# Kernel optimization log

Hardware: AMD Instinct MI355X
Metric: run time of the kernel (lower is better)

The kernel has to match this reference:

```python
import jax, jax.numpy as jnp
import numpy as np

SQRT2 = 1.41421356237
BASE_SCALE = 0.001
CDF_X = 10.0


def erf_poly(x):
    # Abramowitz-Stegun polynomial erf, exactly as the torch source
    sign = jnp.where(x > 0, 1.0, -1.0)  # torch: (x > 0) * 2 - 1
    x = jnp.abs(x)
    a1, a2, a3, a4, a5 = 0.254829592, -0.284496736, 1.421413741, -1.453152027, 1.061405429
    p = 0.3275911
    t = 1.0 / (1.0 + p * x)
    y = 1.0 - ((((a5 * t + a4) * t + a3) * t + a2) * t + a1) * t * jnp.exp(-x * x)
    return sign * y


def rot6d_to_rotmat(x):
    # Zhou et al. 6D rotation: Gram-Schmidt two columns, cross for third
    a1, a2 = x[..., :3], x[..., 3:6]
    b1 = a1 / jnp.linalg.norm(a1, axis=-1, keepdims=True)
    b2 = a2 - jnp.sum(b1 * a2, axis=-1, keepdims=True) * b1
    b2 = b2 / jnp.linalg.norm(b2, axis=-1, keepdims=True)
    b3 = jnp.cross(b1, b2)
    return jnp.stack([b1, b2, b3], axis=-1)  # columns b1,b2,b3 -> [..., 3, 3]


def setup_inputs() -> dict:
    key = jax.random.key(0)
    k1, k2, k3, k4 = jax.random.split(key, 4)
    R, B, G = 65536, 24, 4
    return {
        "w2ls": jax.random.normal(k1, (R, B, 4, 4), dtype=jnp.float32),
        "rays_o": jax.random.normal(k2, (R, 3), dtype=jnp.float32),
        "rays_d": jax.random.normal(k3, (R, 3), dtype=jnp.float32),
        "Gs": jax.random.normal(k4, (B, G, 13), dtype=jnp.float32),
        "N_unique": 1,
    }


def reference(w2ls, rays_o, rays_d, Gs, N_unique):
    # Gs-derived quantities are detached in the original get_1D_gaussians
    Gs = jax.lax.stop_gradient(Gs)
    R = rays_o.shape[0]
    dt = rays_o.dtype

    origins = jnp.concatenate([rays_o, jnp.ones((R, 1), dt)], axis=1)      # [r,4]
    dirs = jnp.concatenate([rays_d, jnp.zeros((R, 1), dt)], axis=1)        # [r,4]
    o = jnp.einsum('rbij,rj->rbi', w2ls, origins)[..., :3]                 # [r,b,3]
    n = jnp.einsum('rbij,rj->rbi', w2ls, dirs)[..., :3]                    # [r,b,3]

    G_mu = Gs[..., 0:3]                                                    # [b,g,3]
    G_std = jnp.abs(Gs[..., 3:6]) + BASE_SCALE                             # [b,g,3]
    G_R = rot6d_to_rotmat(Gs[..., 6:12])                                   # [b,g,3,3]
    G_c = jnp.abs(Gs[..., 12])                                             # [b,g]

    # S = diag(1/std); SR = S @ R scales rows of R
    SR = G_R / G_std[..., None]                                            # [b,g,3,3]
    Sn1 = jnp.einsum('bgki,bgkj->bgij', SR, SR)                            # R^T S^2 R

    mu_d_o = G_mu[None] - o[:, :, None, :]                                 # [r,b,g,3]
    nSn = jnp.einsum('rbi,bgij,rbj->rbg', n, Sn1, n)                       # n^T Sn1 n
    sigma_bar_sqr = 1.0 / nSn                                              # [r,b,g]
    mu_bar = jnp.einsum('rbi,bgij,rbgj->rbg', n, Sn1, mu_d_o) * sigma_bar_sqr
    quad = jnp.einsum('rbgi,bgij,rbgj->rbg', mu_d_o, Sn1, mu_d_o)

    densities = G_c[None] * jnp.exp(-0.5 * (quad - mu_bar ** 2 / sigma_bar_sqr))
    means = mu_bar
    sigmas = jnp.sqrt(sigma_bar_sqr)

    # soft density filter (weights computed on detached means)
    w = jax.nn.sigmoid(100.0 * jax.lax.stop_gradient(means) - 1.0)
    densities = densities * w

    # gaussian1d_cdf at x = 10.0, then shadow map: sum over all (bone, gaussian)
    cdf = densities * 0.5 * (1.0 + erf_poly((CDF_X - means) / (sigmas * SQRT2)))
    shadow_map = jnp.exp(-jnp.sum(cdf, axis=(1, 2)))                       # [r]
    return shadow_map
```

## Files before the change

### kernel.cpp

```cpp
#include <hip/hip_runtime.h>
#include <math.h>


#define NB 24
#define NG 4
#define BASE_SCALE 0.001f

template <int CTRL>
__device__ __forceinline__ float dpp_f(float x) {
    int r = __builtin_amdgcn_update_dpp(0, __float_as_int(x), CTRL, 0xF, 0xF, true);
    return __int_as_float(r);
}

__device__ __forceinline__ float frcp(float x) { return __builtin_amdgcn_rcpf(x); }

__global__ __launch_bounds__(256, 8) void gauss_vis_kernel(
    const float* __restrict__ w2ls,
    const float* __restrict__ rays_o,
    const float* __restrict__ rays_d,
    const float* __restrict__ Gs,
    float* __restrict__ out,
    int R)
{
    __shared__ float4 P[NB * NG * 3];

    const int tid = threadIdx.x;
    const int gid = blockIdx.x * 256 + tid;
    const int ray0 = gid >> 3;
    const int ray = ray0 < R ? ray0 : (R - 1);
    const int oct = tid & 7;
    const int sub = oct & 3;
    const int half = oct >> 2;

    if (tid < NB * NG) {
        const float* gp = Gs + tid * 13;
        float mu0 = gp[0], mu1 = gp[1], mu2 = gp[2];
        float s0 = fabsf(gp[3]) + BASE_SCALE;
        float s1 = fabsf(gp[4]) + BASE_SCALE;
        float s2 = fabsf(gp[5]) + BASE_SCALE;
        float ax = gp[6], ay = gp[7], az = gp[8];
        float bx = gp[9], by = gp[10], bz = gp[11];
        float c = fabsf(gp[12]);
        float inv1 = 1.0f / sqrtf(ax * ax + ay * ay + az * az);
        float b1x = ax * inv1, b1y = ay * inv1, b1z = az * inv1;
        float dot = b1x * bx + b1y * by + b1z * bz;
        float t2x = bx - dot * b1x, t2y = by - dot * b1y, t2z = bz - dot * b1z;
        float inv2 = 1.0f / sqrtf(t2x * t2x + t2y * t2y + t2z * t2z);
        float b2x = t2x * inv2, b2y = t2y * inv2, b2z = t2z * inv2;
        float b3x = b1y * b2z - b1z * b2y;
        float b3y = b1z * b2x - b1x * b2z;
        float b3z = b1x * b2y - b1y * b2x;
        float w0 = 1.0f / (s0 * s0), w1 = 1.0f / (s1 * s1), w2 = 1.0f / (s2 * s2);
        float s00 = b1x * b1x * w0 + b1y * b1y * w1 + b1z * b1z * w2;
        float s01 = b1x * b2x * w0 + b1y * b2y * w1 + b1z * b2z * w2;
        float s02 = b1x * b3x * w0 + b1y * b3y * w1 + b1z * b3z * w2;
        float s11 = b2x * b2x * w0 + b2y * b2y * w1 + b2z * b2z * w2;
        float s12 = b2x * b3x * w0 + b2y * b3y * w1 + b2z * b3z * w2;
        float s22 = b3x * b3x * w0 + b3y * b3y * w1 + b3z * b3z * w2;
        P[tid * 3 + 0] = make_float4(s00, s01, s02, s11);
        P[tid * 3 + 1] = make_float4(s12, s22, mu0, mu1);
        P[tid * 3 + 2] = make_float4(mu2, c, 0.f, 0.f);
    }
    __syncthreads();

    const float rox = rays_o[ray * 3 + 0];
    const float roy = rays_o[ray * 3 + 1];
    const float roz = rays_o[ray * 3 + 2];
    const float rdx = rays_d[ray * 3 + 0];
    const float rdy = rays_d[ray * 3 + 1];
    const float rdz = rays_d[ray * 3 + 2];

    const float4* __restrict__ Wp =
        (const float4*)w2ls + ((size_t)ray * (NB * 4) + half * 4 + sub);
    const int pi0 = (half * NG + sub) * 3;

    float sum = 0.f;
#pragma unroll 2
    for (int k = 0; k < 12; ++k) {
        const float4 M = Wp[k * 8];
        float o_s = fmaf(M.x, rox, fmaf(M.y, roy, fmaf(M.z, roz, M.w)));
        float n_s = fmaf(M.x, rdx, fmaf(M.y, rdy, M.z * rdz));
        float o0 = dpp_f<0x00>(o_s), o1 = dpp_f<0x55>(o_s), o2 = dpp_f<0xAA>(o_s);
        float n0 = dpp_f<0x00>(n_s), n1 = dpp_f<0x55>(n_s), n2 = dpp_f<0xAA>(n_s);

        int pi = pi0 + k * 24;
        float4 p0 = P[pi + 0];
        float4 p1 = P[pi + 1];
        float4 p2 = P[pi + 2];
        float s00 = p0.x, s01 = p0.y, s02 = p0.z, s11 = p0.w;
        float s12 = p1.x, s22 = p1.y;
        float d0 = p1.z - o0, d1 = p1.w - o1, d2 = p2.x - o2;
        float c = p2.y;

        float v0 = s00 * n0 + s01 * n1 + s02 * n2;
        float v1 = s01 * n0 + s11 * n1 + s12 * n2;
        float v2 = s02 * n0 + s12 * n1 + s22 * n2;
        float nSn = v0 * n0 + v1 * n1 + v2 * n2;
        float nSd = v0 * d0 + v1 * d1 + v2 * d2;
        float q0 = s00 * d0 + s01 * d1 + s02 * d2;
        float q1 = s01 * d0 + s11 * d1 + s12 * d2;
        float q2 = s02 * d0 + s12 * d1 + s22 * d2;
        float quad = q0 * d0 + q1 * d1 + q2 * d2;

        float r = __builtin_amdgcn_rsqf(nSn);
        float t = nSd * r;
        float resid = fmaf(t, t, -quad);
        float mean = t * r;

        bool dead = (resid < -28.f) || (mean < -0.15f);
        if (__all(dead)) continue;

        float ew = __expf(1.f - 100.f * mean);
        float denom = 1.f + ew;

        float z = (10.f - mean) * (nSn * r);
        if (!__all(z > 5.f)) {
            float zz = z * z;
            float a = z * fmaf(0.070565992f, zz, 1.5976f);
            denom *= 1.f + __expf(-a);
        }

        float ed = __expf(0.5f * resid);
        sum = fmaf(c * ed, frcp(denom), sum);
    }

    sum += dpp_f<0xB1>(sum);
    sum += dpp_f<0x4E>(sum);
    sum += __shfl_xor(sum, 4, 64);
    if (oct == 0 && ray0 < R) out[ray0] = __expf(-sum);
}

extern "C" void kernel_launch(void* const* d_in, const int* in_sizes, int n_in,
                              void* d_out, int out_size, void* d_ws, size_t ws_size,
                              hipStream_t stream) {
    const float* w2ls   = (const float*)d_in[0];
    const float* rays_o = (const float*)d_in[1];
    const float* rays_d = (const float*)d_in[2];
    const float* Gs     = (const float*)d_in[3];
    float* out = (float*)d_out;

    const int R = in_sizes[1] / 3;
    const int threads = 256;
    const long long total = (long long)R * 8;
    const int blocks = (int)((total + threads - 1) / threads);
    gauss_vis_kernel<<<blocks, threads, 0, stream>>>(w2ls, rays_o, rays_d, Gs, out, R);
}
```

Baseline: 24.42 us.

## Process four rays per 16-lane group with double-buffered register prefetch

```diff
diff --git a/kernel.cpp b/kernel.cpp
--- a/kernel.cpp
+++ b/kernel.cpp
@@ -14,7 +14,9 @@
 
 __device__ __forceinline__ float frcp(float x) { return __builtin_amdgcn_rcpf(x); }
 
-__global__ __launch_bounds__(256, 8) void gauss_vis_kernel(
+struct RayC { float ox, oy, oz, dx, dy, dz; };
+
+__global__ __launch_bounds__(256, 4) void gauss_vis_kernel(
     const float* __restrict__ w2ls,
     const float* __restrict__ rays_o,
     const float* __restrict__ rays_d,
@@ -25,12 +27,6 @@
     __shared__ float4 P[NB * NG * 3];
 
     const int tid = threadIdx.x;
-    const int gid = blockIdx.x * 256 + tid;
-    const int ray0 = gid >> 3;
-    const int ray = ray0 < R ? ray0 : (R - 1);
-    const int oct = tid & 7;
-    const int sub = oct & 3;
-    const int half = oct >> 2;
 
     if (tid < NB * NG) {
         const float* gp = Gs + tid * 13;
@@ -63,71 +59,92 @@
     }
     __syncthreads();
 
-    const float rox = rays_o[ray * 3 + 0];
-    const float roy = rays_o[ray * 3 + 1];
-    const float roz = rays_o[ray * 3 + 2];
-    const float rdx = rays_d[ray * 3 + 0];
-    const float rdy = rays_d[ray * 3 + 1];
-    const float rdz = rays_d[ray * 3 + 2];
+    const int lane16 = tid & 15;
+    const int rsl = (tid & 63) >> 4;
+    const int wid = blockIdx.x * 4 + (tid >> 6);
+    const int Wstride = gridDim.x * 16;
 
-    const float4* __restrict__ Wp =
-        (const float4*)w2ls + ((size_t)ray * (NB * 4) + half * 4 + sub);
-    const int pi0 = (half * NG + sub) * 3;
+    const float4* __restrict__ Wv = (const float4*)w2ls;
+    const int pibase = lane16 * 3;
 
-    float sum = 0.f;
-#pragma unroll 2
-    for (int k = 0; k < 12; ++k) {
-        const float4 M = Wp[k * 8];
-        float o_s = fmaf(M.x, rox, fmaf(M.y, roy, fmaf(M.z, roz, M.w)));
-        float n_s = fmaf(M.x, rdx, fmaf(M.y, rdy, M.z * rdz));
-        float o0 = dpp_f<0x00>(o_s), o1 = dpp_f<0x55>(o_s), o2 = dpp_f<0xAA>(o_s);
-        float n0 = dpp_f<0x00>(n_s), n1 = dpp_f<0x55>(n_s), n2 = dpp_f<0xAA>(n_s);
+    auto loadT = [&](float4 (&M)[6], RayC& rc, int rayt) {
+        int r = rayt < R ? rayt : (R - 1);
+        const float4* __restrict__ p = Wv + (size_t)r * 96 + lane16;
+#pragma unroll
+        for (int k = 0; k < 6; ++k) M[k] = p[k * 16];
+        rc.ox = rays_o[r * 3 + 0]; rc.oy = rays_o[r * 3 + 1]; rc.oz = rays_o[r * 3 + 2];
+        rc.dx = rays_d[r * 3 + 0]; rc.dy = rays_d[r * 3 + 1]; rc.dz = rays_d[r * 3 + 2];
+    };
 
-        int pi = pi0 + k * 24;
-        float4 p0 = P[pi + 0];
-        float4 p1 = P[pi + 1];
-        float4 p2 = P[pi + 2];
-        float s00 = p0.x, s01 = p0.y, s02 = p0.z, s11 = p0.w;
-        float s12 = p1.x, s22 = p1.y;
-        float d0 = p1.z - o0, d1 = p1.w - o1, d2 = p2.x - o2;
-        float c = p2.y;
+    auto compT = [&](const float4 (&M)[6], const RayC& rc, int rayt) {
+        float sum = 0.f;
+#pragma unroll
+        for (int k = 0; k < 6; ++k) {
+            const float4 Mk = M[k];
+            float o_s = fmaf(Mk.x, rc.ox, fmaf(Mk.y, rc.oy, fmaf(Mk.z, rc.oz, Mk.w)));
+            float n_s = fmaf(Mk.x, rc.dx, fmaf(Mk.y, rc.dy, Mk.z * rc.dz));
+            float o0 = dpp_f<0x00>(o_s), o1 = dpp_f<0x55>(o_s), o2 = dpp_f<0xAA>(o_s);
+            float n0 = dpp_f<0x00>(n_s), n1 = dpp_f<0x55>(n_s), n2 = dpp_f<0xAA>(n_s);
 
-        float v0 = s00 * n0 + s01 * n1 + s02 * n2;
-        float v1 = s01 * n0 + s11 * n1 + s12 * n2;
-        float v2 = s02 * n0 + s12 * n1 + s22 * n2;
-        float nSn = v0 * n0 + v1 * n1 + v2 * n2;
-        float nSd = v0 * d0 + v1 * d1 + v2 * d2;
-        float q0 = s00 * d0 + s01 * d1 + s02 * d2;
-        float q1 = s01 * d0 + s11 * d1 + s12 * d2;
-        float q2 = s02 * d0 + s12 * d1 + s22 * d2;
-        float quad = q0 * d0 + q1 * d1 + q2 * d2;
+            int pi = pibase + k * 48;
+            float4 p0 = P[pi + 0];
+            float4 p1 = P[pi + 1];
+            float4 p2 = P[pi + 2];
+            float s00 = p0.x, s01 = p0.y, s02 = p0.z, s11 = p0.w;
+            float s12 = p1.x, s22 = p1.y;
+            float d0 = p1.z - o0, d1 = p1.w - o1, d2 = p2.x - o2;
+            float c = p2.y;
 
-        float r = __builtin_amdgcn_rsqf(nSn);
-        float t = nSd * r;
-        float resid = fmaf(t, t, -quad);
-        float mean = t * r;
+            float v0 = s00 * n0 + s01 * n1 + s02 * n2;
+            float v1 = s01 * n0 + s11 * n1 + s12 * n2;
+            float v2 = s02 * n0 + s12 * n1 + s22 * n2;
+            float nSn = v0 * n0 + v1 * n1 + v2 * n2;
+            float nSd = v0 * d0 + v1 * d1 + v2 * d2;
+            float q0 = s00 * d0 + s01 * d1 + s02 * d2;
+            float q1 = s01 * d0 + s11 * d1 + s12 * d2;
+            float q2 = s02 * d0 + s12 * d1 + s22 * d2;
+            float quad = q0 * d0 + q1 * d1 + q2 * d2;
 
-        bool dead = (resid < -28.f) || (mean < -0.15f);
-        if (__all(dead)) continue;
+            float r = __builtin_amdgcn_rsqf(nSn);
+            float t = nSd * r;
+            float resid = fmaf(t, t, -quad);
+            float mean = t * r;
 
-        float ew = __expf(1.f - 100.f * mean);
-        float denom = 1.f + ew;
-
-        float z = (10.f - mean) * (nSn * r);
-        if (!__all(z > 5.f)) {
+            float ew = __expf(1.f - 100.f * mean);
+            float z = (10.f - mean) * (nSn * r);
             float zz = z * z;
             float a = z * fmaf(0.070565992f, zz, 1.5976f);
-            denom *= 1.f + __expf(-a);
+            float ec = __expf(-a);
+            float denom = (1.f + ew) * (1.f + ec);
+            float ed = __expf(0.5f * resid);
+            sum = fmaf(c * ed, frcp(denom), sum);
         }
+        sum += dpp_f<0xB1>(sum);
+        sum += dpp_f<0x4E>(sum);
+        sum += __shfl_xor(sum, 4, 64);
+        sum += __shfl_xor(sum, 8, 64);
+        if (lane16 == 0 && rayt < R) out[rayt] = __expf(-sum);
+    };
 
-        float ed = __expf(0.5f * resid);
-        sum = fmaf(c * ed, frcp(denom), sum);
-    }
+    const int r0 = wid * 4 + rsl;
+    const int r1 = r0 + Wstride;
+    const int r2 = r1 + Wstride;
+    const int r3 = r2 + Wstride;
 
-    sum += dpp_f<0xB1>(sum);
-    sum += dpp_f<0x4E>(sum);
-    sum += __shfl_xor(sum, 4, 64);
-    if (oct == 0 && ray0 < R) out[ray0] = __expf(-sum);
+    float4 A[6], B[6];
+    RayC Ra, Rb;
+
+    loadT(A, Ra, r0);
+    loadT(B, Rb, r1);
+    __builtin_amdgcn_sched_barrier(0);
+    compT(A, Ra, r0);
+    loadT(A, Ra, r2);
+    __builtin_amdgcn_sched_barrier(0);
+    compT(B, Rb, r1);
+    loadT(B, Rb, r3);
+    __builtin_amdgcn_sched_barrier(0);
+    compT(A, Ra, r2);
+    compT(B, Rb, r3);
 }
 
 extern "C" void kernel_launch(void* const* d_in, const int* in_sizes, int n_in,
@@ -141,7 +158,6 @@
 
     const int R = in_sizes[1] / 3;
     const int threads = 256;
-    const long long total = (long long)R * 8;
-    const int blocks = (int)((total + threads - 1) / threads);
+    const int blocks = (R + 63) / 64;
     gauss_vis_kernel<<<blocks, threads, 0, stream>>>(w2ls, rays_o, rays_d, Gs, out, R);
 }
```

New measurement: 24.87 us. Within noise of the previous version (+1.9%).

## Use Cholesky factor of precision matrix and branchless exp2 evaluation

Applied to the files above, without the earlier changes.

```diff
diff --git a/kernel.cpp b/kernel.cpp
--- a/kernel.cpp
+++ b/kernel.cpp
@@ -13,6 +13,7 @@
 }
 
 __device__ __forceinline__ float frcp(float x) { return __builtin_amdgcn_rcpf(x); }
+__device__ __forceinline__ float fexp2(float x) { return __builtin_amdgcn_exp2f(x); }
 
 __global__ __launch_bounds__(256, 8) void gauss_vis_kernel(
     const float* __restrict__ w2ls,
@@ -57,8 +58,15 @@
         float s11 = b2x * b2x * w0 + b2y * b2y * w1 + b2z * b2z * w2;
         float s12 = b2x * b3x * w0 + b2y * b3y * w1 + b2z * b3z * w2;
         float s22 = b3x * b3x * w0 + b3y * b3y * w1 + b3z * b3z * w2;
-        P[tid * 3 + 0] = make_float4(s00, s01, s02, s11);
-        P[tid * 3 + 1] = make_float4(s12, s22, mu0, mu1);
+        float u00 = sqrtf(fmaxf(s00, 1e-20f));
+        float iu00 = 1.0f / u00;
+        float u01 = s01 * iu00;
+        float u02 = s02 * iu00;
+        float u11 = sqrtf(fmaxf(s11 - u01 * u01, 1e-20f));
+        float u12 = (s12 - u01 * u02) / u11;
+        float u22 = sqrtf(fmaxf(s22 - u02 * u02 - u12 * u12, 1e-20f));
+        P[tid * 3 + 0] = make_float4(u00, u01, u02, u11);
+        P[tid * 3 + 1] = make_float4(u12, u22, mu0, mu1);
         P[tid * 3 + 2] = make_float4(mu2, c, 0.f, 0.f);
     }
     __syncthreads();
@@ -87,40 +95,33 @@
         float4 p0 = P[pi + 0];
         float4 p1 = P[pi + 1];
         float4 p2 = P[pi + 2];
-        float s00 = p0.x, s01 = p0.y, s02 = p0.z, s11 = p0.w;
-        float s12 = p1.x, s22 = p1.y;
+        float u00 = p0.x, u01 = p0.y, u02 = p0.z, u11 = p0.w;
+        float u12 = p1.x, u22 = p1.y;
         float d0 = p1.z - o0, d1 = p1.w - o1, d2 = p2.x - o2;
         float c = p2.y;
 
-        float v0 = s00 * n0 + s01 * n1 + s02 * n2;
-        float v1 = s01 * n0 + s11 * n1 + s12 * n2;
-        float v2 = s02 * n0 + s12 * n1 + s22 * n2;
-        float nSn = v0 * n0 + v1 * n1 + v2 * n2;
-        float nSd = v0 * d0 + v1 * d1 + v2 * d2;
-        float q0 = s00 * d0 + s01 * d1 + s02 * d2;
-        float q1 = s01 * d0 + s11 * d1 + s12 * d2;
-        float q2 = s02 * d0 + s12 * d1 + s22 * d2;
-        float quad = q0 * d0 + q1 * d1 + q2 * d2;
+        float un0 = fmaf(u02, n2, fmaf(u01, n1, u00 * n0));
+        float un1 = fmaf(u12, n2, u11 * n1);
+        float un2 = u22 * n2;
+        float ud0 = fmaf(u02, d2, fmaf(u01, d1, u00 * d0));
+        float ud1 = fmaf(u12, d2, u11 * d1);
+        float ud2 = u22 * d2;
+
+        float nSn = fmaf(un2, un2, fmaf(un1, un1, un0 * un0));
+        float nSd = fmaf(un2, ud2, fmaf(un1, ud1, un0 * ud0));
+        float quad = fmaf(ud2, ud2, fmaf(ud1, ud1, ud0 * ud0));
 
         float r = __builtin_amdgcn_rsqf(nSn);
         float t = nSd * r;
         float resid = fmaf(t, t, -quad);
-        float mean = t * r;
 
-        bool dead = (resid < -28.f) || (mean < -0.15f);
-        if (__all(dead)) continue;
+        float ed = fexp2(0.72134752f * resid);
+        float ew = fexp2(fmaf(t * r, -144.26950f, 1.4426950f));
+        float z = r * fmaf(nSn, 10.f, -nSd);
+        float zz = z * z;
+        float ec = fexp2(-z * fmaf(0.10180843f, zz, 2.3048389f));
 
-        float ew = __expf(1.f - 100.f * mean);
-        float denom = 1.f + ew;
-
-        float z = (10.f - mean) * (nSn * r);
-        if (!__all(z > 5.f)) {
-            float zz = z * z;
-            float a = z * fmaf(0.070565992f, zz, 1.5976f);
-            denom *= 1.f + __expf(-a);
-        }
-
-        float ed = __expf(0.5f * resid);
+        float denom = (1.f + ew) * (1.f + ec);
         sum = fmaf(c * ed, frcp(denom), sum);
     }
 
```

Measured after the change: 22.45 us. 8.1% less time.
